# Optimization experiments

Measured on AMD Instinct MI355X. Metric: run time of the kernel, lower is better.

Reference implementation:

```python
import jax, jax.numpy as jnp
import numpy as np
from math import atanh

B, T, D_IN, H = 16, 1024, 512, 1024
INIT_A = atanh(0.95)


def setup_inputs() -> dict:
    key = jax.random.key(0)
    k1, k2, k3, k4 = jax.random.split(key, 4)
    x = jax.random.normal(k1, (B, T, D_IN), dtype=jnp.float32)
    h0 = jax.random.normal(k2, (B, H), dtype=jnp.float32)
    # raw_a initialized near atanh(0.95) as in the module, with small jitter
    raw_a = INIT_A + 0.01 * jax.random.normal(k3, (H,), dtype=jnp.float32)
    # xavier-uniform for W_x.weight [H, D_IN]
    limit = float(np.sqrt(6.0 / (D_IN + H)))
    W = jax.random.uniform(k4, (H, D_IN), dtype=jnp.float32, minval=-limit, maxval=limit)
    b = jnp.zeros((H,), dtype=jnp.float32)
    return {"x": x, "h0": h0, "raw_a": raw_a, "W": W, "b": b}


def reference(x, h0, raw_a, W, b):
    # h_t = a * h_{t-1} + W x_t + b, computed via cumprod/cumsum parallel-scan trick
    a = jnp.tanh(raw_a)                                   # [H] (rho is None)
    z = jnp.einsum('btd,hd->bth', x, W) + b               # [B,T,H]
    A = jnp.broadcast_to(a, (x.shape[1], a.shape[0]))     # [T,H]
    p = jnp.cumprod(A, axis=0)[None]                      # [1,T,H], p[t] = a^(t+1)
    v = jnp.cumsum(z / jnp.maximum(p, 1e-12), axis=1)     # [B,T,H]
    h = v * p + p * h0[:, None, :]                        # include initial state
    zero_mask = (jnp.abs(a) < 1e-6)[None, None, :]        # degenerate a ~ 0 channels
    h = jnp.where(zero_mask, z, h)
    return h
```

## Files before the change

### kernel.cpp

```cpp
#include <hip/hip_runtime.h>
#include <cstdint>

#define B_DIM 16
#define T_DIM 1024
#define DK    512
#define H_DIM 1024

#define TCH    128
#define NCH    (T_DIM / TCH)
#define NB     128
#define NSTRIP (H_DIM / NB)
#define NKT    16

typedef __bf16 bf16x8 __attribute__((ext_vector_type(8)));
typedef __bf16 bf16x4 __attribute__((ext_vector_type(4)));
typedef float  f32x4  __attribute__((ext_vector_type(4)));

typedef __attribute__((address_space(1))) unsigned int* as1p;
typedef __attribute__((address_space(3))) unsigned int* as3p;

__device__ __forceinline__ void async_cp16(const void* g, void* l) {
  __builtin_amdgcn_global_load_lds((as1p)(uint64_t)g,
                                   (as3p)(uint32_t)(uint64_t)l, 16, 0, 0);
}

__global__ __launch_bounds__(256) void prep(const float* __restrict__ W,
                                            __bf16* __restrict__ wbT,
                                            const float* __restrict__ raw_a,
                                            float4* __restrict__ meta,
                                            unsigned long long* __restrict__ flags) {
  const int bid = blockIdx.x, tid = threadIdx.x;
  if (bid < 512) {
    const int i = bid * 256 + tid;
    const int h  = i >> 7;
    const int k0 = (i & 127) * 4;
    f32x4 v = ((const f32x4*)W)[i];
    bf16x4 o;
    o.x = (__bf16)v.x; o.y = (__bf16)v.y; o.z = (__bf16)v.z; o.w = (__bf16)v.w;
    *(bf16x4*)(wbT + ((size_t)(k0 >> 3) * H_DIM + h) * 8 + (k0 & 7)) = o;
  } else if (bid < 516) {
    const int h = (bid - 512) * 256 + tid;
    const float a = tanhf(raw_a[h]);
    const float la2 = log2f(fabsf(a));
    meta[h] = make_float4(a, la2, (a < 0.f) ? 1.f : 0.f, (fabsf(a) < 1e-6f) ? 1.f : 0.f);
  } else {
    flags[(bid - 516) * 256 + tid] = 0ULL;
  }
}

__global__ __launch_bounds__(256, 3) void fused_rnn(
    const float* __restrict__ xf,
    const __bf16* __restrict__ wbT,
    const float* __restrict__ bias,
    const float4* __restrict__ meta,
    const float* __restrict__ h0g,
    unsigned long long* __restrict__ flags,
    float* __restrict__ out) {
  __shared__ __align__(16) float  Asf[2][8][TCH][4];
  __shared__ __align__(16) __bf16 Bs[2][4][NB][8];
  __shared__ float chunkTot[2][NB];
  __shared__ float colCarry[NB];

  const int tid  = threadIdx.x;
  const int wave = tid >> 6;
  const int lane = tid & 63;
  const int q  = lane >> 4;
  const int c  = lane & 15;
  const int rw = wave & 1;
  const int cg = wave >> 1;

  const int bid   = blockIdx.x;
  const int g     = bid & 127;
  const int strip = bid >> 7;
  const int b     = g >> 3;
  const int chunk = g & 7;
  const int t0    = chunk * TCH;
  const int n0    = strip * NB;

  float bias_j[4];
#pragma unroll
  for (int j = 0; j < 4; ++j) bias_j[j] = bias[n0 + cg * 64 + j * 16 + c];

  const float* const xB = xf + (size_t)(b * T_DIM + t0) * DK;

  auto stage = [&](int kt, int buf) {
#pragma unroll
    for (int it = 0; it < 4; ++it) {
      const int s = it * 256 + tid;
      const int kq4 = s >> 7, row = s & 127;
      async_cp16(xB + (size_t)row * DK + kt * 32 + kq4 * 4,
                 &Asf[buf][kq4][row][0]);
    }
#pragma unroll
    for (int it = 0; it < 2; ++it) {
      const int s = it * 256 + tid;
      const int kq = s >> 7, col = s & 127;
      async_cp16(wbT + ((size_t)(kt * 4 + kq) * H_DIM + n0 + col) * 8,
                 &Bs[buf][kq][col][0]);
    }
  };

  f32x4 acc[4][4];
#pragma unroll
  for (int i = 0; i < 4; ++i)
#pragma unroll
    for (int j = 0; j < 4; ++j)
      acc[i][j] = (f32x4){bias_j[j], bias_j[j], bias_j[j], bias_j[j]};

  stage(0, 0); stage(1, 1);

  for (int kt = 0; kt < NKT; ++kt) {
    const int buf = kt & 1;
    if (kt < NKT - 1) asm volatile("s_waitcnt vmcnt(6)" ::: "memory");
    else              asm volatile("s_waitcnt vmcnt(0)" ::: "memory");
    __builtin_amdgcn_s_barrier();
    bf16x8 af[4], bfr[4];
#pragma unroll
    for (int i = 0; i < 4; ++i) {
      const int row = rw * 64 + i * 16 + c;
      const f32x4 a0 = *(const f32x4*)(&Asf[buf][2 * q][row][0]);
      const f32x4 a1 = *(const f32x4*)(&Asf[buf][2 * q + 1][row][0]);
      bf16x8 t;
      t[0] = (__bf16)a0.x; t[1] = (__bf16)a0.y; t[2] = (__bf16)a0.z; t[3] = (__bf16)a0.w;
      t[4] = (__bf16)a1.x; t[5] = (__bf16)a1.y; t[6] = (__bf16)a1.z; t[7] = (__bf16)a1.w;
      af[i] = t;
    }
#pragma unroll
    for (int j = 0; j < 4; ++j)
      bfr[j] = *(const bf16x8*)(&Bs[buf][q][cg * 64 + j * 16 + c][0]);
#pragma unroll
    for (int i = 0; i < 4; ++i)
#pragma unroll
      for (int j = 0; j < 4; ++j)
        acc[i][j] = __builtin_amdgcn_mfma_f32_16x16x32_bf16(af[i], bfr[j], acc[i][j], 0, 0, 0);
    __builtin_amdgcn_sched_barrier(0);
    __builtin_amdgcn_s_barrier();
    if (kt < NKT - 2) stage(kt + 2, buf);
  }

  float la2_j[4], a_j[4], ai_j[4], sgn_j[4], h0_j[4];
  bool zm_j[4];
#pragma unroll
  for (int j = 0; j < 4; ++j) {
    const int col = n0 + cg * 64 + j * 16 + c;
    const float4 mt = meta[col];
    a_j[j]   = mt.x;
    la2_j[j] = mt.y;
    ai_j[j]  = 1.f / mt.x;
    sgn_j[j] = (mt.z != 0.f) ? -1.f : 1.f;
    zm_j[j]  = mt.w != 0.f;
    h0_j[j]  = h0g[(size_t)b * H_DIM + col];
  }

  float base_[4][4];
  float icarry[4] = {0.f, 0.f, 0.f, 0.f};
#pragma unroll
  for (int i = 0; i < 4; ++i) {
    const int tp10 = t0 + rw * 64 + i * 16 + q * 4 + 1;
#pragma unroll
    for (int j = 0; j < 4; ++j) {
      float u = __builtin_amdgcn_exp2f(-la2_j[j] * (float)tp10) * sgn_j[j];
      f32x4 wv;
#pragma unroll
      for (int r = 0; r < 4; ++r) {
        const float uu = fminf(u, 1e12f);
        const float inv = (u < 0.f) ? 1e12f : uu;
        wv[r] = acc[i][j][r] * inv;
        u *= ai_j[j];
      }
      const float pr0 = wv[0];
      const float pr1 = pr0 + wv[1];
      const float pr2 = pr1 + wv[2];
      const float pr3 = pr2 + wv[3];
      const float x1 = __shfl_xor(pr3, 16, 64);
      const float x2 = __shfl_xor(pr3, 32, 64);
      const float x3 = __shfl_xor(pr3, 48, 64);
      float sq = 0.f;
      if (q >= 2) sq += x2 + x3;
      if (q & 1) sq += x1;
      const float base = icarry[j] + sq;
      base_[i][j] = base;
      acc[i][j] = (f32x4){base + pr0, base + pr1, base + pr2, base + pr3};
      icarry[j] += pr3 + x1 + x2 + x3;
    }
  }
  if (q == 0) {
#pragma unroll
    for (int j = 0; j < 4; ++j) chunkTot[rw][cg * 64 + j * 16 + c] = icarry[j];
  }
  __syncthreads();

  if (tid < NB) {
    const int col = tid;
    const size_t fb = ((size_t)b * NSTRIP + strip) * NCH * NB;
    const float tot = chunkTot[0][col] + chunkTot[1][col];
    atomicExch(&flags[fb + (size_t)chunk * NB + col],
               (1ULL << 32) | (unsigned long long)__float_as_uint(tot));
    float s = 0.f;
    for (int p = 0; p < chunk; ++p) {
      unsigned long long v = atomicAdd(&flags[fb + (size_t)p * NB + col], 0ULL);
      while (!(v >> 32)) {
        __builtin_amdgcn_s_sleep(4);
        v = atomicAdd(&flags[fb + (size_t)p * NB + col], 0ULL);
      }
      s += __uint_as_float((unsigned int)v);
    }
    colCarry[col] = s;
  }
  __syncthreads();

  float cc_[4];
#pragma unroll
  for (int j = 0; j < 4; ++j) {
    const int colL = cg * 64 + j * 16 + c;
    float s = colCarry[colL];
    if (rw) s += chunkTot[0][colL];
    cc_[j] = s + h0_j[j];
  }
#pragma unroll
  for (int i = 0; i < 4; ++i) {
    const int tp10 = t0 + rw * 64 + i * 16 + q * 4 + 1;
#pragma unroll
    for (int j = 0; j < 4; ++j) {
      float pv = __builtin_amdgcn_exp2f(la2_j[j] * (float)tp10) * sgn_j[j];
      const int col = n0 + cg * 64 + j * 16 + c;
#pragma unroll
      for (int r = 0; r < 4; ++r) {
        const int tl = t0 + rw * 64 + i * 16 + q * 4 + r;
        const float hv = pv * (acc[i][j][r] + cc_[j]);
        const float wr = acc[i][j][r] - ((r == 0) ? base_[i][j] : acc[i][j][r - 1]);
        out[(size_t)(b * T_DIM + tl) * H_DIM + col] = zm_j[j] ? wr * 1e-12f : hv;
        pv *= a_j[j];
      }
    }
  }
}

extern "C" void kernel_launch(void* const* d_in, const int* in_sizes, int n_in,
                              void* d_out, int out_size, void* d_ws, size_t ws_size,
                              hipStream_t stream) {
  const float* x     = (const float*)d_in[0];
  const float* h0    = (const float*)d_in[1];
  const float* raw_a = (const float*)d_in[2];
  const float* W     = (const float*)d_in[3];
  const float* bias  = (const float*)d_in[4];
  float* out = (float*)d_out;

  char* ws = (char*)d_ws;
  __bf16* wbT = (__bf16*)(ws);
  float4* meta = (float4*)(ws + 1048576);
  unsigned long long* flags =
      (unsigned long long*)(ws + 1048576 + 16384);

  prep<<<1028, 256, 0, stream>>>(W, wbT, raw_a, meta, flags);
  fused_rnn<<<1024, 256, 0, stream>>>(x, wbT, bias, meta, h0, flags, out);
}
```

Measured before the change: 145.9 us.

## Stage x as bf16 in LDS via registers, triple-buffer W, raise occupancy

The x tile is now loaded into registers, converted to bf16 and written to LDS, instead of being copied asynchronously as fp32 and converted after the LDS read. This halves the A-tile LDS footprint. The W tile becomes triple-buffered, and the epilogue scratch arrays reuse the A buffer. Together these cut LDS per block enough to raise launch bounds to 4 blocks per CU, so all 1024 blocks can be resident at once, which also helps the cross-chunk flag spin-wait. The cost is more VGPR use and compiler-managed waits on the register-staged loads.

Measured after the change: 139.7 us. 1.04x faster.

```diff
diff --git a/kernel.cpp b/kernel.cpp
--- a/kernel.cpp
+++ b/kernel.cpp
@@ -48,7 +48,7 @@
   }
 }
 
-__global__ __launch_bounds__(256, 3) void fused_rnn(
+__global__ __launch_bounds__(256, 4) void fused_rnn(
     const float* __restrict__ xf,
     const __bf16* __restrict__ wbT,
     const float* __restrict__ bias,
@@ -56,10 +56,9 @@
     const float* __restrict__ h0g,
     unsigned long long* __restrict__ flags,
     float* __restrict__ out) {
-  __shared__ __align__(16) float  Asf[2][8][TCH][4];
-  __shared__ __align__(16) __bf16 Bs[2][4][NB][8];
-  __shared__ float chunkTot[2][NB];
-  __shared__ float colCarry[NB];
+  __shared__ __align__(16) __bf16 As[2][4][TCH][8];
+  __shared__ __align__(16) __bf16 Bs[3][4][NB][8];
+  float* const scr = (float*)&As[0][0][0][0];
 
   const int tid  = threadIdx.x;
   const int wave = tid >> 6;
@@ -77,20 +76,31 @@
   const int t0    = chunk * TCH;
   const int n0    = strip * NB;
 
+  const int t8 = tid >> 3;
+  const int ck = tid & 7;
+
   float bias_j[4];
 #pragma unroll
   for (int j = 0; j < 4; ++j) bias_j[j] = bias[n0 + cg * 64 + j * 16 + c];
 
   const float* const xB = xf + (size_t)(b * T_DIM + t0) * DK;
 
-  auto stage = [&](int kt, int buf) {
+  f32x4 ar[4];
+  auto loadA = [&](int kt) {
+#pragma unroll
+    for (int it = 0; it < 4; ++it)
+      ar[it] = *(const f32x4*)(xB + (size_t)(it * 32 + t8) * DK + kt * 32 + ck * 4);
+  };
+  auto writeA = [&](int buf) {
 #pragma unroll
     for (int it = 0; it < 4; ++it) {
-      const int s = it * 256 + tid;
-      const int kq4 = s >> 7, row = s & 127;
-      async_cp16(xB + (size_t)row * DK + kt * 32 + kq4 * 4,
-                 &Asf[buf][kq4][row][0]);
-    }
+      bf16x4 o;
+      o.x = (__bf16)ar[it].x; o.y = (__bf16)ar[it].y;
+      o.z = (__bf16)ar[it].z; o.w = (__bf16)ar[it].w;
+      *(bf16x4*)(&As[buf][ck >> 1][it * 32 + t8][(ck & 1) * 4]) = o;
+    }
+  };
+  auto stageB = [&](int kt, int buf) {
 #pragma unroll
     for (int it = 0; it < 2; ++it) {
       const int s = it * 256 + tid;
@@ -107,27 +117,27 @@
     for (int j = 0; j < 4; ++j)
       acc[i][j] = (f32x4){bias_j[j], bias_j[j], bias_j[j], bias_j[j]};
 
-  stage(0, 0); stage(1, 1);
+  loadA(0);
+  stageB(0, 0); stageB(1, 1); stageB(2, 2);
+  writeA(0);
+  loadA(1);
+  writeA(1);
+  loadA(2);
 
   for (int kt = 0; kt < NKT; ++kt) {
-    const int buf = kt & 1;
-    if (kt < NKT - 1) asm volatile("s_waitcnt vmcnt(6)" ::: "memory");
+    const int bufA = kt & 1, bufB = kt % 3;
+    if (kt < NKT - 2) asm volatile("s_waitcnt vmcnt(6)" ::: "memory");
     else              asm volatile("s_waitcnt vmcnt(0)" ::: "memory");
+    asm volatile("s_waitcnt lgkmcnt(0)" ::: "memory");
     __builtin_amdgcn_s_barrier();
+
     bf16x8 af[4], bfr[4];
 #pragma unroll
-    for (int i = 0; i < 4; ++i) {
-      const int row = rw * 64 + i * 16 + c;
-      const f32x4 a0 = *(const f32x4*)(&Asf[buf][2 * q][row][0]);
-      const f32x4 a1 = *(const f32x4*)(&Asf[buf][2 * q + 1][row][0]);
-      bf16x8 t;
-      t[0] = (__bf16)a0.x; t[1] = (__bf16)a0.y; t[2] = (__bf16)a0.z; t[3] = (__bf16)a0.w;
-      t[4] = (__bf16)a1.x; t[5] = (__bf16)a1.y; t[6] = (__bf16)a1.z; t[7] = (__bf16)a1.w;
-      af[i] = t;
-    }
+    for (int i = 0; i < 4; ++i)
+      af[i] = *(const bf16x8*)(&As[bufA][q][rw * 64 + i * 16 + c][0]);
 #pragma unroll
     for (int j = 0; j < 4; ++j)
-      bfr[j] = *(const bf16x8*)(&Bs[buf][q][cg * 64 + j * 16 + c][0]);
+      bfr[j] = *(const bf16x8*)(&Bs[bufB][q][cg * 64 + j * 16 + c][0]);
 #pragma unroll
     for (int i = 0; i < 4; ++i)
 #pragma unroll
@@ -135,7 +145,10 @@
         acc[i][j] = __builtin_amdgcn_mfma_f32_16x16x32_bf16(af[i], bfr[j], acc[i][j], 0, 0, 0);
     __builtin_amdgcn_sched_barrier(0);
     __builtin_amdgcn_s_barrier();
-    if (kt < NKT - 2) stage(kt + 2, buf);
+    __builtin_amdgcn_sched_barrier(0);
+    if (kt + 3 < NKT) stageB(kt + 3, bufB);
+    if (kt + 2 < NKT) writeA(bufA);
+    if (kt + 3 < NKT) loadA(kt + 3);
   }
 
   float la2_j[4], a_j[4], ai_j[4], sgn_j[4], h0_j[4];
@@ -186,14 +199,14 @@
   }
   if (q == 0) {
 #pragma unroll
-    for (int j = 0; j < 4; ++j) chunkTot[rw][cg * 64 + j * 16 + c] = icarry[j];
+    for (int j = 0; j < 4; ++j) scr[rw * NB + cg * 64 + j * 16 + c] = icarry[j];
   }
   __syncthreads();
 
   if (tid < NB) {
     const int col = tid;
     const size_t fb = ((size_t)b * NSTRIP + strip) * NCH * NB;
-    const float tot = chunkTot[0][col] + chunkTot[1][col];
+    const float tot = scr[col] + scr[NB + col];
     atomicExch(&flags[fb + (size_t)chunk * NB + col],
                (1ULL << 32) | (unsigned long long)__float_as_uint(tot));
     float s = 0.f;
@@ -205,7 +218,7 @@
       }
       s += __uint_as_float((unsigned int)v);
     }
-    colCarry[col] = s;
+    scr[2 * NB + col] = s;
   }
   __syncthreads();
 
@@ -213,8 +226,8 @@
 #pragma unroll
   for (int j = 0; j < 4; ++j) {
     const int colL = cg * 64 + j * 16 + c;
-    float s = colCarry[colL];
-    if (rw) s += chunkTot[0][colL];
+    float s = scr[2 * NB + colL];
+    if (rw) s += scr[colL];
     cc_[j] = s + h0_j[j];
   }
 #pragma unroll
```
